# Kernel tuning notes

Hardware: AMD Instinct MI355X
Metric: run time of the kernel (lower is better)

Reference implementation:

```python
import jax, jax.numpy as jnp
import numpy as np

K, PAD, POOL = 3, 1, 2

def _conv_block(x, w, b):
    # x: [B,C,H,W]; w: [O, C*K*K] (Linear weight, feature order (C,kh,kw)); b: [O]
    O = w.shape[0]
    C = x.shape[1]
    ker = w.reshape(O, C, K, K)  # OIHW, matches torch unfold+linear ordering
    y = jax.lax.conv_general_dilated(
        x, ker, window_strides=(1, 1), padding=[(PAD, PAD), (PAD, PAD)],
        dimension_numbers=("NCHW", "OIHW", "NCHW"))
    y = y + b[None, :, None, None]
    y = jax.nn.relu(y)
    # non-overlapping max pool, drops remainder like torch unfold (sizes divisible here)
    y = jax.lax.reduce_window(y, -jnp.inf, jax.lax.max,
                              (1, 1, POOL, POOL), (1, 1, POOL, POOL), "VALID")
    return y

def setup_inputs() -> dict:
    key = jax.random.key(0)
    ks = jax.random.split(key, 9)
    B, Cin, H = 64, 3, 128
    C1, C2, FC, NCLS = 64, 128, 256, 1000
    flat = C2 * (H // 4) * (H // 4)  # 128*32*32 = 131072
    s = 0.05
    return {
        "x": jax.random.normal(ks[0], (B, Cin, H, H), jnp.float32),
        "conv1_w": jax.random.normal(ks[1], (C1, Cin * K * K), jnp.float32) * s,
        "conv1_b": jax.random.normal(ks[2], (C1,), jnp.float32) * s,
        "conv2_w": jax.random.normal(ks[3], (C2, C1 * K * K), jnp.float32) * s,
        "conv2_b": jax.random.normal(ks[4], (C2,), jnp.float32) * s,
        "fc1_w": jax.random.normal(ks[5], (FC, flat), jnp.float32) * 0.005,
        "fc1_b": jax.random.normal(ks[6], (FC,), jnp.float32) * s,
        "fc2_w": jax.random.normal(ks[7], (NCLS, FC), jnp.float32) * s,
        "fc2_b": jax.random.normal(ks[8], (NCLS,), jnp.float32) * s,
    }

def reference(x, conv1_w, conv1_b, conv2_w, conv2_b, fc1_w, fc1_b, fc2_w, fc2_b):
    h = _conv_block(x, conv1_w, conv1_b)      # [B,64,64,64]
    h = _conv_block(h, conv2_w, conv2_b)      # [B,128,32,32]
    h = h.reshape(h.shape[0], -1)             # NCHW flatten, same as torch .view
    h = jax.nn.relu(h @ fc1_w.T + fc1_b)
    return h @ fc2_w.T + fc2_b                # [B,1000]
```

## Files before the change

### kernel.cpp

```cpp
#include <hip/hip_runtime.h>
#include <hip/hip_bf16.h>

typedef __attribute__((ext_vector_type(8))) short short8;
typedef __attribute__((ext_vector_type(4))) float f32x4;
typedef __attribute__((ext_vector_type(16))) float f32x16;

#define KFC   131072
#define NCLS  1000

__device__ __forceinline__ unsigned short f2bf(float f) {
  union { float f; unsigned u; } v; v.f = f;
  unsigned r = v.u + 0x7FFFu + ((v.u >> 16) & 1u);
  return (unsigned short)(r >> 16);
}

__device__ __forceinline__ unsigned pk2bf(float a, float b) {
  __hip_bfloat162 h = __float22bfloat162_rn(float2{a, b});
  union { __hip_bfloat162 h; unsigned u; } c; c.h = h;
  return c.u;
}

__global__ __launch_bounds__(256) void prep_w1(
    const float* __restrict__ w1, short* __restrict__ Bp1) {
  int i = blockIdx.x * 256 + threadIdx.x;
  int o = i >> 5, k = i & 31;
  Bp1[i] = (k < 27) ? (short)f2bf(w1[o * 27 + k]) : (short)0;
}

__global__ __launch_bounds__(256) void conv1_mfma(
    const float* __restrict__ x, const short* __restrict__ Bp1,
    const float* __restrict__ b1, unsigned short* __restrict__ y) {
  __shared__ unsigned short tile[1152];
  const int t = threadIdx.x;
  const int blk = blockIdx.x;
  const int tx = blk & 7, ty = (blk >> 3) & 7, b = blk >> 6;
  const int w = t >> 6, lane = t & 63;
  const int l15 = lane & 15, lg = lane >> 4;

  const int ih0 = ty * 16 - 1, iw0 = tx * 16 - 1;
  for (int i = t; i < 1152; i += 256) {
    unsigned short v = 0;
    if (i < 1080) {
      int ci = i / 360, rem = i - ci * 360;
      int tr = rem / 20, tc = rem - tr * 20;
      int ih = ih0 + tr, iw = iw0 + tc;
      if (tc < 18 && (unsigned)ih < 128u && (unsigned)iw < 128u)
        v = f2bf(x[(b * 3 + ci) * 16384 + (ih << 7) + iw]);
    }
    tile[i] = v;
  }

  short8 bf[4];
#pragma unroll
  for (int n = 0; n < 4; ++n)
    bf[n] = *(const short8*)(Bp1 + ((n * 16 + l15) << 5) + (lg << 3));

  int soff[8];
#pragma unroll
  for (int j = 0; j < 8; ++j) {
    int k = lg * 8 + j;
    if (k < 27) {
      int ci = k / 9, rem = k - ci * 9;
      int r = rem / 3, s = rem - r * 3;
      soff[j] = ci * 360 + r * 20 + s + l15 + w * 80;
    } else {
      soff[j] = 1080;
    }
  }
  __syncthreads();

  f32x4 acc[4][4];
#pragma unroll
  for (int m = 0; m < 4; ++m)
#pragma unroll
    for (int n = 0; n < 4; ++n) acc[m][n] = (f32x4){0.f, 0.f, 0.f, 0.f};

#pragma unroll
  for (int m = 0; m < 4; ++m) {
    union { short8 s; unsigned short u[8]; } af;
#pragma unroll
    for (int j = 0; j < 8; ++j) af.u[j] = tile[soff[j] + m * 20];
#pragma unroll
    for (int n = 0; n < 4; ++n)
      acc[m][n] = __builtin_amdgcn_mfma_f32_16x16x32_bf16(af.s, bf[n], acc[m][n], 0, 0, 0);
  }

#pragma unroll
  for (int n = 0; n < 4; ++n) {
    const int o = n * 16 + l15;
    const float bias = b1[o];
#pragma unroll
    for (int q = 0; q < 2; ++q) {
      const int pr = ty * 8 + w * 2 + q;
      float v0 = fmaxf(fmaxf(acc[2 * q][n][0], acc[2 * q][n][1]),
                       fmaxf(acc[2 * q + 1][n][0], acc[2 * q + 1][n][1]));
      float v1 = fmaxf(fmaxf(acc[2 * q][n][2], acc[2 * q][n][3]),
                       fmaxf(acc[2 * q + 1][n][2], acc[2 * q + 1][n][3]));
      v0 = fmaxf(v0 + bias, 0.f);
      v1 = fmaxf(v1 + bias, 0.f);
      const int pc = tx * 8 + lg * 2;
      unsigned short* dst = y + ((((size_t)b << 6) + pr) << 12) + ((size_t)pc << 6) + o;
      dst[0]  = f2bf(v0);
      dst[64] = f2bf(v1);
    }
  }
}

__global__ __launch_bounds__(256) void prep_w2(
    const float* __restrict__ w2, short* __restrict__ Bp) {
  int i = blockIdx.x * 256 + threadIdx.x;
  int c = i & 15, o = (i >> 4) & 127, q = i >> 11;
  int pos = q >> 2, c4 = q & 3;
  int ch = c4 * 16 + c;
  Bp[i] = (short)f2bf(w2[o * 576 + ch * 9 + pos]);
}

__global__ __launch_bounds__(256) void conv2_mfma(
    const short* __restrict__ yin, const short* __restrict__ Bp,
    const float* __restrict__ b2, unsigned int* __restrict__ A32) {
  __shared__ short tile[180 * 72];
  const int t = threadIdx.x;
  const int blk = blockIdx.x;
  const int tx = blk & 3, ty = (blk >> 2) & 7, b = blk >> 5;
  const int w = t >> 6, lane = t & 63;
  const int l31 = lane & 31, h = lane >> 5;

  const int ih0 = ty * 8 - 1, iw0 = tx * 16 - 1;

  for (int i = t; i < 1440; i += 256) {
    int p = i >> 3, q8 = i & 7;
    int sy = p / 18, sx = p - sy * 18;
    int ih = ih0 + sy, iw = iw0 + sx;
    short8 v = (short8){0, 0, 0, 0, 0, 0, 0, 0};
    if (((unsigned)ih < 64u) && ((unsigned)iw < 64u))
      v = *(const short8*)(yin + ((((size_t)b << 6) + ih) << 12) + ((size_t)iw << 6) + q8 * 8);
    *(short8*)&tile[p * 72 + q8 * 8] = v;
  }
  __syncthreads();

  f32x16 acc[4];
#pragma unroll
  for (int s = 0; s < 4; ++s)
#pragma unroll
    for (int j = 0; j < 16; ++j) acc[s][j] = 0.f;

  const int arow = l31 >> 4;
  const int acol = l31 & 15;
  const int chof = h * 8;
  const int obase = w * 32 + l31;

  short8 afb[2][4];
  short8 bfb[2];

#pragma unroll
  for (int s = 0; s < 4; ++s)
    afb[0][s] = *(const short8*)&tile[((2 * s + arow) * 18 + acol) * 72 + chof];
  bfb[0] = *(const short8*)(Bp + (size_t)obase * 16 + chof);

#pragma unroll
  for (int q = 0; q < 36; ++q) {
    if (q < 35) {
      const int nq = q + 1, npos = nq >> 2, nc4 = nq & 3;
      const int nkh = npos / 3, nkw = npos - nkh * 3;
#pragma unroll
      for (int s = 0; s < 4; ++s)
        afb[nq & 1][s] = *(const short8*)&tile[((2 * s + arow + nkh) * 18 + acol + nkw) * 72 + nc4 * 16 + chof];
      bfb[nq & 1] = *(const short8*)(Bp + (size_t)(nq * 128 + obase) * 16 + chof);
    }
#pragma unroll
    for (int s = 0; s < 4; ++s)
      acc[s] = __builtin_amdgcn_mfma_f32_32x32x16_bf16(afb[q & 1][s], bfb[q & 1], acc[s], 0, 0, 0);
  }

  const size_t bbase = ((size_t)b << 16);
  const float bias = b2[obase];
#pragma unroll
  for (int s = 0; s < 4; ++s) {
    const int prow = ty * 4 + s;
    float v0 = fmaxf(fmaxf(acc[s][0], acc[s][1]), fmaxf(acc[s][8],  acc[s][9]));
    float v1 = fmaxf(fmaxf(acc[s][2], acc[s][3]), fmaxf(acc[s][10], acc[s][11]));
    float v2 = fmaxf(fmaxf(acc[s][4], acc[s][5]), fmaxf(acc[s][12], acc[s][13]));
    float v3 = fmaxf(fmaxf(acc[s][6], acc[s][7]), fmaxf(acc[s][14], acc[s][15]));
    v0 = fmaxf(v0 + bias, 0.f);
    v1 = fmaxf(v1 + bias, 0.f);
    v2 = fmaxf(v2 + bias, 0.f);
    v3 = fmaxf(v3 + bias, 0.f);
    unsigned int* dst = A32 + bbase + (size_t)obase * 512 + prow * 16 + tx * 4 + h;
    dst[0] = (unsigned)f2bf(v0) | ((unsigned)f2bf(v1) << 16);
    dst[2] = (unsigned)f2bf(v2) | ((unsigned)f2bf(v3) << 16);
  }
}

__global__ __launch_bounds__(256) void fc1_mfma(
    const unsigned short* __restrict__ A, const float* __restrict__ W,
    float* __restrict__ P) {
  __shared__ short Al[64][520];
  const int t = threadIdx.x;
  const int blk = blockIdx.x;
  const int kc = blk >> 1, nt = blk & 1;
  const int wn = t >> 6, lane = t & 63;
  const int l15 = lane & 15, lg = lane >> 4;

  {
    const int row = t >> 2, q = t & 3;
    const unsigned short* asrc = A + (size_t)row * KFC + kc * 512 + q * 128;
    short8 ar[16];
#pragma unroll
    for (int i = 0; i < 16; ++i) ar[i] = *(const short8*)(asrc + i * 8);
#pragma unroll
    for (int i = 0; i < 16; ++i) *(short8*)&Al[row][q * 128 + i * 8] = ar[i];
  }
  __syncthreads();

  f32x4 acc[4][2];
#pragma unroll
  for (int m = 0; m < 4; ++m)
#pragma unroll
    for (int n = 0; n < 2; ++n) acc[m][n] = (f32x4){0.f, 0.f, 0.f, 0.f};

  const float* wrow[2];
#pragma unroll
  for (int n = 0; n < 2; ++n)
    wrow[n] = W + (size_t)(nt * 128 + wn * 32 + n * 16 + l15) * KFC + kc * 512 + lg * 8;

#pragma unroll
  for (int ks = 0; ks < 16; ++ks) {
    short8 bf[2];
#pragma unroll
    for (int n = 0; n < 2; ++n) {
      f32x4 u = *(const f32x4*)(wrow[n] + ks * 32);
      f32x4 v = *(const f32x4*)(wrow[n] + ks * 32 + 4);
      union { short8 s; unsigned u32[4]; } pk;
      pk.u32[0] = pk2bf(u[0], u[1]);
      pk.u32[1] = pk2bf(u[2], u[3]);
      pk.u32[2] = pk2bf(v[0], v[1]);
      pk.u32[3] = pk2bf(v[2], v[3]);
      bf[n] = pk.s;
    }
    short8 af[4];
#pragma unroll
    for (int m = 0; m < 4; ++m)
      af[m] = *(const short8*)&Al[m * 16 + l15][ks * 32 + lg * 8];
#pragma unroll
    for (int n = 0; n < 2; ++n)
#pragma unroll
      for (int m = 0; m < 4; ++m)
        acc[m][n] = __builtin_amdgcn_mfma_f32_16x16x32_bf16(af[m], bf[n], acc[m][n], 0, 0, 0);
  }

  float* dst = P + (size_t)kc * 16384;
#pragma unroll
  for (int m = 0; m < 4; ++m)
#pragma unroll
    for (int n = 0; n < 2; ++n)
#pragma unroll
      for (int j = 0; j < 4; ++j) {
        int brow = m * 16 + lg * 4 + j;
        int o = nt * 128 + wn * 32 + n * 16 + l15;
        dst[brow * 256 + o] = acc[m][n][j];
      }
}

__global__ __launch_bounds__(256) void fc1_reduce_kernel(
    const float* __restrict__ P, const float* __restrict__ fb1,
    float* __restrict__ Y) {
  __shared__ float red[4][64];
  const int t = threadIdx.x;
  const int iq = t & 63, pg = t >> 6;
  const int gidx = blockIdx.x * 64 + iq;
  const float* p0 = P + (size_t)(pg * 64) * 16384 + gidx;
  float s0 = 0, s1 = 0, s2 = 0, s3 = 0;
  for (int p = 0; p < 64; p += 4) {
    s0 += p0[(size_t)(p + 0) * 16384];
    s1 += p0[(size_t)(p + 1) * 16384];
    s2 += p0[(size_t)(p + 2) * 16384];
    s3 += p0[(size_t)(p + 3) * 16384];
  }
  red[pg][iq] = (s0 + s1) + (s2 + s3);
  __syncthreads();
  if (pg == 0) {
    float tot = (red[0][iq] + red[1][iq]) + (red[2][iq] + red[3][iq]);
    Y[gidx] = fmaxf(tot + fb1[gidx & 255], 0.f);
  }
}

__global__ __launch_bounds__(256) void fc2_kernel(
    const float* __restrict__ Y, const float* __restrict__ W2,
    const float* __restrict__ b2, float* __restrict__ out) {
  int tid = blockIdx.x * 256 + threadIdx.x;
  if (tid >= 64 * NCLS) return;
  int b = tid / NCLS, n = tid - b * NCLS;
  const float4* yv = (const float4*)(Y + b * 256);
  const float4* wv = (const float4*)(W2 + n * 256);
  float acc = 0.f;
#pragma unroll 8
  for (int f = 0; f < 64; ++f) {
    float4 a = yv[f], w = wv[f];
    acc += a.x * w.x + a.y * w.y + a.z * w.z + a.w * w.w;
  }
  out[tid] = acc + b2[n];
}

extern "C" void kernel_launch(void* const* d_in, const int* in_sizes, int n_in,
                              void* d_out, int out_size, void* d_ws, size_t ws_size,
                              hipStream_t stream) {
  const float* x   = (const float*)d_in[0];
  const float* w1  = (const float*)d_in[1];
  const float* b1  = (const float*)d_in[2];
  const float* w2  = (const float*)d_in[3];
  const float* b2  = (const float*)d_in[4];
  const float* fw1 = (const float*)d_in[5];
  const float* fb1 = (const float*)d_in[6];
  const float* fw2 = (const float*)d_in[7];
  const float* fb2 = (const float*)d_in[8];
  float* out = (float*)d_out;

  unsigned short* Y1 = (unsigned short*)d_ws;
  unsigned short* A16 = Y1 + 16777216;
  short* Bp = (short*)(A16 + 8388608);
  short* Bp1 = Bp + 73728;
  float* P  = (float*)(Bp1 + 2048);
  float* Yf = P + 4194304;

  prep_w2<<<288, 256, 0, stream>>>(w2, Bp);
  prep_w1<<<8, 256, 0, stream>>>(w1, Bp1);
  conv1_mfma<<<4096, 256, 0, stream>>>(x, Bp1, b1, Y1);
  conv2_mfma<<<2048, 256, 0, stream>>>((const short*)Y1, Bp, b2, (unsigned int*)A16);
  fc1_mfma<<<512, 256, 0, stream>>>(A16, fw1, P);
  fc1_reduce_kernel<<<256, 256, 0, stream>>>(P, fb1, Yf);
  fc2_kernel<<<250, 256, 0, stream>>>(Yf, fw2, fb2, out);
}
```

Before: 117.0 us.

## Reuse conv2 LDS row fragments across kh and merge weight prep kernels

The conv2 inner loop is reorganized so each (channel group, kw) step loads 9 input-row fragments once and reuses them across the three kh taps and four output rows. This cuts LDS reads from 4 per MFMA group to 9 per 12 MFMAs. It also fuses the two weight-prep kernels into one launch to save launch overhead. The cost is more live registers (double-buffered 9+3 short8 fragments), which may lower occupancy.

```diff
diff --git a/kernel.cpp b/kernel.cpp
--- a/kernel.cpp
+++ b/kernel.cpp
@@ -20,11 +20,19 @@
   return c.u;
 }
 
-__global__ __launch_bounds__(256) void prep_w1(
-    const float* __restrict__ w1, short* __restrict__ Bp1) {
+__global__ __launch_bounds__(256) void prep_w(
+    const float* __restrict__ w2, const float* __restrict__ w1,
+    short* __restrict__ Bp, short* __restrict__ Bp1) {
   int i = blockIdx.x * 256 + threadIdx.x;
-  int o = i >> 5, k = i & 31;
-  Bp1[i] = (k < 27) ? (short)f2bf(w1[o * 27 + k]) : (short)0;
+  if (i < 73728) {
+    int c = i & 15, o = (i >> 4) & 127, q = i >> 11;
+    int pos = q >> 2, c4 = q & 3;
+    Bp[i] = (short)f2bf(w2[o * 576 + (c4 * 16 + c) * 9 + pos]);
+  } else if (i < 75776) {
+    int j = i - 73728;
+    int o = j >> 5, k = j & 31;
+    Bp1[j] = (k < 27) ? (short)f2bf(w1[o * 27 + k]) : (short)0;
+  }
 }
 
 __global__ __launch_bounds__(256) void conv1_mfma(
@@ -106,15 +114,6 @@
   }
 }
 
-__global__ __launch_bounds__(256) void prep_w2(
-    const float* __restrict__ w2, short* __restrict__ Bp) {
-  int i = blockIdx.x * 256 + threadIdx.x;
-  int c = i & 15, o = (i >> 4) & 127, q = i >> 11;
-  int pos = q >> 2, c4 = q & 3;
-  int ch = c4 * 16 + c;
-  Bp[i] = (short)f2bf(w2[o * 576 + ch * 9 + pos]);
-}
-
 __global__ __launch_bounds__(256) void conv2_mfma(
     const short* __restrict__ yin, const short* __restrict__ Bp,
     const float* __restrict__ b2, unsigned int* __restrict__ A32) {
@@ -149,27 +148,34 @@
   const int chof = h * 8;
   const int obase = w * 32 + l31;
 
-  short8 afb[2][4];
-  short8 bfb[2];
-
-#pragma unroll
-  for (int s = 0; s < 4; ++s)
-    afb[0][s] = *(const short8*)&tile[((2 * s + arow) * 18 + acol) * 72 + chof];
-  bfb[0] = *(const short8*)(Bp + (size_t)obase * 16 + chof);
-
-#pragma unroll
-  for (int q = 0; q < 36; ++q) {
-    if (q < 35) {
-      const int nq = q + 1, npos = nq >> 2, nc4 = nq & 3;
-      const int nkh = npos / 3, nkw = npos - nkh * 3;
+  short8 rcb[2][9];
+  short8 bfb[2][3];
+
+#pragma unroll
+  for (int j = 0; j < 9; ++j)
+    rcb[0][j] = *(const short8*)&tile[((j + arow) * 18 + acol) * 72 + chof];
+#pragma unroll
+  for (int kh = 0; kh < 3; ++kh)
+    bfb[0][kh] = *(const short8*)(Bp + (size_t)((kh * 3) * 4 * 128 + obase) * 16 + chof);
+
+#pragma unroll
+  for (int it = 0; it < 12; ++it) {
+    const int c4 = it / 3, kw = it - 3 * c4;
+    (void)c4; (void)kw;
+    if (it < 11) {
+      const int nit = it + 1, nc4 = nit / 3, nkw = nit - 3 * nc4;
+#pragma unroll
+      for (int j = 0; j < 9; ++j)
+        rcb[nit & 1][j] = *(const short8*)&tile[((j + arow) * 18 + acol + nkw) * 72 + nc4 * 16 + chof];
+#pragma unroll
+      for (int kh = 0; kh < 3; ++kh)
+        bfb[nit & 1][kh] = *(const short8*)(Bp + (size_t)((((kh * 3 + nkw) * 4 + nc4) * 128) + obase) * 16 + chof);
+    }
+#pragma unroll
+    for (int kh = 0; kh < 3; ++kh)
 #pragma unroll
       for (int s = 0; s < 4; ++s)
-        afb[nq & 1][s] = *(const short8*)&tile[((2 * s + arow + nkh) * 18 + acol + nkw) * 72 + nc4 * 16 + chof];
-      bfb[nq & 1] = *(const short8*)(Bp + (size_t)(nq * 128 + obase) * 16 + chof);
-    }
-#pragma unroll
-    for (int s = 0; s < 4; ++s)
-      acc[s] = __builtin_amdgcn_mfma_f32_32x32x16_bf16(afb[q & 1][s], bfb[q & 1], acc[s], 0, 0, 0);
+        acc[s] = __builtin_amdgcn_mfma_f32_32x32x16_bf16(rcb[it & 1][2 * s + kh], bfb[it & 1][kh], acc[s], 0, 0, 0);
   }
 
   const size_t bbase = ((size_t)b << 16);
@@ -322,8 +328,7 @@
   float* P  = (float*)(Bp1 + 2048);
   float* Yf = P + 4194304;
 
-  prep_w2<<<288, 256, 0, stream>>>(w2, Bp);
-  prep_w1<<<8, 256, 0, stream>>>(w1, Bp1);
+  prep_w<<<296, 256, 0, stream>>>(w2, w1, Bp, Bp1);
   conv1_mfma<<<4096, 256, 0, stream>>>(x, Bp1, b1, Y1);
   conv2_mfma<<<2048, 256, 0, stream>>>((const short*)Y1, Bp, b2, (unsigned int*)A16);
   fc1_mfma<<<512, 256, 0, stream>>>(A16, fw1, P);
```

Result: slower. 132.7 us (+13.4%).
